# Kernel tuning notes

Measured on AMD Instinct MI355X. Metric: run time of the kernel, lower is better.

## Reference

```python
import jax, jax.numpy as jnp
import numpy as np

B, N, P2, D, L, K = 256, 256, 64, 128, 2, 9  # batch, nodes, patch^2, embed_dim, vig blocks, knn edges
FFN = 4 * D


def _ln(x, g, b, eps=1e-5):
    m = jnp.mean(x, -1, keepdims=True)
    v = jnp.mean((x - m) ** 2, -1, keepdims=True)
    return (x - m) / jnp.sqrt(v + eps) * g + b


def _lrelu(x):
    return jnp.where(x >= 0, x, 0.01 * x)


def _vig_block(x, mask, mf, fc1_w, fc1_b, conv_w, conv_b, fc2_w, fc2_b, f1_w, f1_b, f2_w, f2_b):
    # Grapher: fc1 -> dynamic kNN -> max-relative graph conv -> fc2, residual
    sc = x
    h = x @ fc1_w + fc1_b  # [B,N,D]
    # pairwise squared distances in feature space; masked nodes excluded as neighbors
    x2 = jnp.sum(h * h, -1)
    d2 = x2[:, :, None] + x2[:, None, :] - 2.0 * jnp.einsum('bnd,bmd->bnm', h, h)
    d2 = jnp.where(mask[:, None, :], d2, 1e10)
    _, idx = jax.lax.top_k(-d2, K)  # [B,N,K] nearest-neighbor indices (non-diff)
    Bq, Nq, Dq = h.shape
    hj = jnp.take_along_axis(h, idx.reshape(Bq, Nq * K, 1), axis=1).reshape(Bq, Nq, K, Dq)
    vj = jnp.take_along_axis(mask, idx.reshape(Bq, Nq * K), axis=1).reshape(Bq, Nq, K)
    rel = jnp.where(vj[..., None], hj - h[:, :, None, :], -1e9)
    mrel = jnp.where(vj.any(2)[..., None], rel.max(2), 0.0)  # max-relative aggregation
    h = _lrelu(jnp.concatenate([h, mrel], -1) @ conv_w + conv_b)
    x = (h @ fc2_w + fc2_b) + sc
    # FFN, residual (drop_path = identity at eval)
    sc = x
    x = _lrelu(x @ f1_w + f1_b) @ f2_w + f2_b + sc
    return x * mf


def setup_inputs() -> dict:
    key = jax.random.key(0)
    ks = jax.random.split(key, 32)
    s = 0.02
    d = {
        'nodes_batch': jax.random.normal(ks[0], (B, N, P2), jnp.float32),
        'node_mask': jax.random.randint(ks[1], (B, N), 0, 2) > 0,
        'emb_w1': jax.random.normal(ks[2], (P2, 2 * D), jnp.float32) * s,
        'emb_b1': jnp.zeros((2 * D,), jnp.float32),
        'emb_ln1_g': jnp.ones((2 * D,), jnp.float32),
        'emb_ln1_b': jnp.zeros((2 * D,), jnp.float32),
        'emb_w2': jax.random.normal(ks[3], (2 * D, D), jnp.float32) * s,
        'emb_b2': jnp.zeros((D,), jnp.float32),
        'emb_ln2_g': jnp.ones((D,), jnp.float32),
        'emb_ln2_b': jnp.zeros((D,), jnp.float32),
        'vig_fc1_w': jax.random.normal(ks[4], (L, D, D), jnp.float32) * s,
        'vig_fc1_b': jnp.zeros((L, D), jnp.float32),
        'vig_conv_w': jax.random.normal(ks[5], (L, 2 * D, D), jnp.float32) * s,
        'vig_conv_b': jnp.zeros((L, D), jnp.float32),
        'vig_fc2_w': jax.random.normal(ks[6], (L, D, D), jnp.float32) * s,
        'vig_fc2_b': jnp.zeros((L, D), jnp.float32),
        'vig_ffn1_w': jax.random.normal(ks[7], (L, D, FFN), jnp.float32) * s,
        'vig_ffn1_b': jnp.zeros((L, FFN), jnp.float32),
        'vig_ffn2_w': jax.random.normal(ks[8], (L, FFN, D), jnp.float32) * s,
        'vig_ffn2_b': jnp.zeros((L, D), jnp.float32),
        'out_w1': jax.random.normal(ks[9], (D, 512), jnp.float32) * s,
        'out_b1': jnp.zeros((512,), jnp.float32),
        'out_w2': jax.random.normal(ks[10], (512, 2048), jnp.float32) * s,
        'out_b2': jnp.zeros((2048,), jnp.float32),
    }
    return d


def reference(nodes_batch, node_mask, emb_w1, emb_b1, emb_ln1_g, emb_ln1_b, emb_w2, emb_b2,
              emb_ln2_g, emb_ln2_b, vig_fc1_w, vig_fc1_b, vig_conv_w, vig_conv_b,
              vig_fc2_w, vig_fc2_b, vig_ffn1_w, vig_ffn1_b, vig_ffn2_w, vig_ffn2_b,
              out_w1, out_b1, out_w2, out_b2):
    mf = node_mask[..., None].astype(nodes_batch.dtype)  # [B,N,1]
    # node embed MLP
    x = _lrelu(_ln(nodes_batch @ emb_w1 + emb_b1, emb_ln1_g, emb_ln1_b))
    x = _ln(x @ emb_w2 + emb_b2, emb_ln2_g, emb_ln2_b)
    x = x * mf
    for l in range(L):
        x = _vig_block(x, node_mask, mf,
                       vig_fc1_w[l], vig_fc1_b[l], vig_conv_w[l], vig_conv_b[l],
                       vig_fc2_w[l], vig_fc2_b[l], vig_ffn1_w[l], vig_ffn1_b[l],
                       vig_ffn2_w[l], vig_ffn2_b[l])
    # masked mean pool
    sum_feat = (x * mf).sum(1)
    num_feat = jnp.maximum(mf.sum(1), 1.0)
    g = sum_feat / num_feat
    return _lrelu(g @ out_w1 + out_b1) @ out_w2 + out_b2
```

## Files before the change

kernel.cpp:

```cpp
#include <hip/hip_runtime.h>
#include <cstdint>

#define BB    256
#define NNODE 256
#define PP2   64
#define DD    128
#define LLAY  2
#define KNN   9
#define FFND  512
#define BNROWS (BB*NNODE)

#define LRELU_(v) ((v) >= 0.f ? (v) : 0.01f*(v))

enum { ACT_NONE = 0, ACT_LRELU = 1 };

typedef short  short8_t  __attribute__((ext_vector_type(8)));
typedef float  f32x4     __attribute__((ext_vector_type(4)));
typedef unsigned short us4 __attribute__((ext_vector_type(4)));
typedef unsigned short us8 __attribute__((ext_vector_type(8)));

__device__ inline unsigned short f2bf(float x) {
    unsigned u = __float_as_uint(x);
    unsigned r = (u + 0x7FFFu + ((u >> 16) & 1u)) >> 16;
    return (unsigned short)r;
}
__device__ inline float bf2f(unsigned short h) {
    return __uint_as_float(((unsigned)h) << 16);
}

__device__ inline void gload16(const void* src, void* dst) {
    __builtin_amdgcn_global_load_lds(
        (const __attribute__((address_space(1))) void*)src,
        (__attribute__((address_space(3))) void*)dst, 16, 0, 0);
}

template<int ROWS, int WAVES>
__device__ inline void stage64g(const unsigned short* __restrict__ g, size_t rowbase,
                                int Kel, int k0, unsigned short* lds, int w, int lane)
{
    constexpr int PER = (ROWS*128/1024) / WAVES;
    #pragma unroll
    for (int i = 0; i < PER; ++i) {
        const int inst = w + i*WAVES;
        const unsigned o  = (unsigned)inst*1024u + (unsigned)lane*16u;
        const int      r  = (int)(o >> 7);
        const unsigned cb = o & 127u;
        const unsigned cs = cb ^ ((unsigned)(r & 7) << 4);
        gload16((const char*)(g + (rowbase + (size_t)r)*(size_t)Kel + k0) + cs,
                (char*)lds + (size_t)inst*1024u);
    }
}

__device__ inline short8_t frag64(const unsigned short* lds, int r, int cb) {
    return *reinterpret_cast<const short8_t*>(
        (const char*)lds + (size_t)r*128 + (unsigned)(cb ^ ((r & 7) << 4)));
}

__device__ inline us8 read8sw(const unsigned short* lds, int r, unsigned cb) {
    return *reinterpret_cast<const us8*>(
        (const char*)lds + (size_t)r*128 + (cb ^ ((unsigned)(r & 7) << 4)));
}

__device__ inline unsigned grp16_min_u32(unsigned v) {
    unsigned t;
    t = (unsigned)__builtin_amdgcn_update_dpp(-1, (int)v, 0xB1,  0xF, 0xF, false); v = t < v ? t : v;
    t = (unsigned)__builtin_amdgcn_update_dpp(-1, (int)v, 0x4E,  0xF, 0xF, false); v = t < v ? t : v;
    t = (unsigned)__builtin_amdgcn_update_dpp(-1, (int)v, 0x124, 0xF, 0xF, false); v = t < v ? t : v;
    t = (unsigned)__builtin_amdgcn_update_dpp(-1, (int)v, 0x128, 0xF, 0xF, false); v = t < v ? t : v;
    return v;
}

__device__ inline float dpp_rowsum16(float v) {
    float t;
    t = __uint_as_float((unsigned)__builtin_amdgcn_update_dpp(0, (int)__float_as_uint(v), 0x111, 0xF, 0xF, false)); v += t;
    t = __uint_as_float((unsigned)__builtin_amdgcn_update_dpp(0, (int)__float_as_uint(v), 0x112, 0xF, 0xF, false)); v += t;
    t = __uint_as_float((unsigned)__builtin_amdgcn_update_dpp(0, (int)__float_as_uint(v), 0x114, 0xF, 0xF, false)); v += t;
    t = __uint_as_float((unsigned)__builtin_amdgcn_update_dpp(0, (int)__float_as_uint(v), 0x118, 0xF, 0xF, false)); v += t;
    return v;
}

#define WAITB0  { asm volatile("s_waitcnt vmcnt(0)" ::: "memory");  __builtin_amdgcn_s_barrier(); asm volatile("" ::: "memory"); }
#define WAITB2  { asm volatile("s_waitcnt vmcnt(2)" ::: "memory");  __builtin_amdgcn_s_barrier(); asm volatile("" ::: "memory"); }
#define WAITB4  { asm volatile("s_waitcnt vmcnt(4)" ::: "memory");  __builtin_amdgcn_s_barrier(); asm volatile("" ::: "memory"); }
#define WAITB2L { asm volatile("s_waitcnt vmcnt(2) lgkmcnt(0)" ::: "memory"); __builtin_amdgcn_s_barrier(); asm volatile("" ::: "memory"); }

template<int ACT, bool RES, bool MASK, bool OUTF, bool OUTB, bool OUTS>
__global__ __launch_bounds__(256)
void bgemm_k(const unsigned short* __restrict__ A,
             const unsigned short* __restrict__ W,
             const float* __restrict__ bias,
             const float* __restrict__ resp,
             const int* __restrict__ mask,
             float* __restrict__ Cf, unsigned short* __restrict__ Cb,
             unsigned short* Ohi, unsigned short* Olo,
             int M, int N, int K)
{
    __shared__ __align__(16) unsigned short As[128*64];
    __shared__ __align__(16) unsigned short Bs[128*64];

    const int tid  = threadIdx.x;
    const int lane = tid & 63;
    const int w    = tid >> 6;
    const int wr   = w >> 1, wc = w & 1;
    const int row0 = blockIdx.x * 128;
    const int col0 = blockIdx.y * 128;
    const int l15  = lane & 15;
    const int ko   = lane >> 4;

    f32x4 acc[4][4];
    #pragma unroll
    for (int m = 0; m < 4; ++m)
        #pragma unroll
        for (int n = 0; n < 4; ++n) acc[m][n] = (f32x4){0.f,0.f,0.f,0.f};

    for (int k0 = 0; k0 < K; k0 += 64) {
        stage64g<128,4>(A, (size_t)row0, K, k0, As, w, lane);
        stage64g<128,4>(W, (size_t)col0, K, k0, Bs, w, lane);
        __syncthreads();
        #pragma unroll
        for (int ks = 0; ks < 2; ++ks) {
            short8_t aF[4], bF[4];
            #pragma unroll
            for (int m = 0; m < 4; ++m)
                aF[m] = frag64(As, wr*64 + m*16 + l15, ks*64 + ko*16);
            #pragma unroll
            for (int n = 0; n < 4; ++n)
                bF[n] = frag64(Bs, wc*64 + n*16 + l15, ks*64 + ko*16);
            #pragma unroll
            for (int m = 0; m < 4; ++m)
                #pragma unroll
                for (int n = 0; n < 4; ++n)
                    acc[m][n] = __builtin_amdgcn_mfma_f32_16x16x32_bf16(aF[m], bF[n], acc[m][n], 0, 0, 0);
        }
        __syncthreads();
    }

    #pragma unroll
    for (int m = 0; m < 4; ++m) {
        const int rbase = row0 + wr*64 + m*16 + ko*4;
        #pragma unroll
        for (int n = 0; n < 4; ++n) {
            const int col = col0 + wc*64 + n*16 + l15;
            const float bv = bias[col];
            #pragma unroll
            for (int r = 0; r < 4; ++r) {
                const int row = rbase + r;
                float v = acc[m][n][r] + bv;
                if constexpr (ACT == ACT_LRELU) v = LRELU_(v);
                if constexpr (RES)  v += resp[(size_t)row*N + col];
                if constexpr (MASK) v *= (mask[row] != 0) ? 1.f : 0.f;
                if constexpr (OUTF) Cf[(size_t)row*N + col] = v;
                if constexpr (OUTB) Cb[(size_t)row*N + col] = f2bf(v);
                if constexpr (OUTS) {
                    unsigned short h = f2bf(v);
                    Ohi[(size_t)row*N + col] = h;
                    Olo[(size_t)row*N + col] = f2bf(v - bf2f(h));
                }
            }
        }
    }
}

template<int WR, int WC, bool DO_LRELU, bool MASKMUL, int MODE, bool AF32>
__global__ __launch_bounds__(WR*WC*64)
void bgemm_ln_k(const void* __restrict__ Ap,
                const unsigned short* __restrict__ W,
                const float* __restrict__ bias,
                const float* __restrict__ gam,
                const float* __restrict__ bet,
                const int* __restrict__ mask,
                void* __restrict__ outv,
                unsigned short* __restrict__ ohi, unsigned short* __restrict__ olo,
                int K)
{
    constexpr int BM = WR*64;
    constexpr int BN = WC*64;
    constexpr int THREADS = WR*WC*64;
    constexpr int WAVES = THREADS/64;
    __shared__ __align__(16) unsigned short As[BM*64];
    __shared__ __align__(16) unsigned short Bs[BN*64];
    __shared__ float red_s[WC][BM];
    __shared__ float red_q[WC][BM];
    __shared__ float mu_l[BM];
    __shared__ float rs_l[BM];

    const int tid  = threadIdx.x;
    const int lane = tid & 63;
    const int w    = tid >> 6;
    const int wr   = w / WC, wc = w % WC;
    const int row0 = blockIdx.x * BM;
    const int l15  = lane & 15;
    const int ko   = lane >> 4;

    f32x4 acc[4][4];
    #pragma unroll
    for (int m = 0; m < 4; ++m)
        #pragma unroll
        for (int n = 0; n < 4; ++n) acc[m][n] = (f32x4){0.f,0.f,0.f,0.f};

    for (int k0 = 0; k0 < K; k0 += 64) {
        if constexpr (AF32) {
            const float* Af = (const float*)Ap;
            constexpr int CH = (BM*8)/THREADS;
            #pragma unroll
            for (int i = 0; i < CH; ++i) {
                const int q = i*THREADS + tid;
                const unsigned o  = (unsigned)q*16u;
                const int      r  = (int)(o >> 7);
                const unsigned cb = o & 127u;
                const unsigned cs = cb ^ ((unsigned)(r & 7) << 4);
                const float* src = Af + (size_t)(row0 + r)*K + k0 + (cs >> 1);
                const float4 f0 = *reinterpret_cast<const float4*>(src);
                const float4 f1 = *reinterpret_cast<const float4*>(src + 4);
                short8_t v;
                v[0]=(short)f2bf(f0.x); v[1]=(short)f2bf(f0.y); v[2]=(short)f2bf(f0.z); v[3]=(short)f2bf(f0.w);
                v[4]=(short)f2bf(f1.x); v[5]=(short)f2bf(f1.y); v[6]=(short)f2bf(f1.z); v[7]=(short)f2bf(f1.w);
                *reinterpret_cast<short8_t*>((char*)As + o) = v;
            }
        } else {
            stage64g<BM,WAVES>((const unsigned short*)Ap, (size_t)row0, K, k0, As, w, lane);
        }
        stage64g<BN,WAVES>(W, 0, K, k0, Bs, w, lane);
        __syncthreads();
        #pragma unroll
        for (int ks = 0; ks < 2; ++ks) {
            short8_t aF[4], bF[4];
            #pragma unroll
            for (int m = 0; m < 4; ++m)
                aF[m] = frag64(As, wr*64 + m*16 + l15, ks*64 + ko*16);
            #pragma unroll
            for (int n = 0; n < 4; ++n)
                bF[n] = frag64(Bs, wc*64 + n*16 + l15, ks*64 + ko*16);
            #pragma unroll
            for (int m = 0; m < 4; ++m)
                #pragma unroll
                for (int n = 0; n < 4; ++n)
                    acc[m][n] = __builtin_amdgcn_mfma_f32_16x16x32_bf16(aF[m], bF[n], acc[m][n], 0, 0, 0);
        }
        __syncthreads();
    }

    float bv[4];
    #pragma unroll
    for (int n = 0; n < 4; ++n) bv[n] = bias[wc*64 + n*16 + l15];
    #pragma unroll
    for (int m = 0; m < 4; ++m)
        #pragma unroll
        for (int n = 0; n < 4; ++n)
            #pragma unroll
            for (int r = 0; r < 4; ++r) acc[m][n][r] += bv[n];

    #pragma unroll
    for (int m = 0; m < 4; ++m) {
        #pragma unroll
        for (int r = 0; r < 4; ++r) {
            float s = acc[m][0][r] + acc[m][1][r] + acc[m][2][r] + acc[m][3][r];
            float q = acc[m][0][r]*acc[m][0][r] + acc[m][1][r]*acc[m][1][r]
                    + acc[m][2][r]*acc[m][2][r] + acc[m][3][r]*acc[m][3][r];
            s = dpp_rowsum16(s);
            q = dpp_rowsum16(q);
            if (l15 == 15) {
                int rl = wr*64 + m*16 + ko*4 + r;
                red_s[wc][rl] = s;
                red_q[wc][rl] = q;
            }
        }
    }
    __syncthreads();
    if (tid < BM) {
        float s = 0.f, q = 0.f;
        #pragma unroll
        for (int c2 = 0; c2 < WC; ++c2) { s += red_s[c2][tid]; q += red_q[c2][tid]; }
        float mu  = s * (1.0f/BN);
        float var = q * (1.0f/BN) - mu*mu;
        mu_l[tid] = mu;
        rs_l[tid] = rsqrtf(fmaxf(var, 0.f) + 1e-5f);
    }
    __syncthreads();

    float gm[4], bt[4];
    #pragma unroll
    for (int n = 0; n < 4; ++n) {
        int col = wc*64 + n*16 + l15;
        gm[n] = gam[col]; bt[n] = bet[col];
    }
    #pragma unroll
    for (int m = 0; m < 4; ++m) {
        #pragma unroll
        for (int r = 0; r < 4; ++r) {
            const int rl  = wr*64 + m*16 + ko*4 + r;
            const int row = row0 + rl;
            const float mu = mu_l[rl], rs = rs_l[rl];
            float mf = 1.f;
            if constexpr (MASKMUL) mf = (mask[row] != 0) ? 1.f : 0.f;
            #pragma unroll
            for (int n = 0; n < 4; ++n) {
                const int col = wc*64 + n*16 + l15;
                float y = (acc[m][n][r] - mu) * rs * gm[n] + bt[n];
                if constexpr (DO_LRELU) y = LRELU_(y);
                if constexpr (MASKMUL)  y *= mf;
                if constexpr (MODE == 1) {
                    ((unsigned short*)outv)[(size_t)row*BN + col] = f2bf(y);
                } else {
                    unsigned short h = f2bf(y);
                    ohi[(size_t)row*BN + col] = h;
                    olo[(size_t)row*BN + col] = f2bf(y - bf2f(h));
                }
            }
        }
    }
}

__global__ __launch_bounds__(1024)
void fc1_dist_topk_gather_k(const unsigned short* __restrict__ xhi,
                            const unsigned short* __restrict__ xlo,
                            const unsigned short* __restrict__ Whi,
                            const unsigned short* __restrict__ Wlo,
                            const float* __restrict__ fc1b,
                            const int* __restrict__ mask,
                            unsigned short* __restrict__ cat)
{
    __shared__ __align__(16) unsigned short BUF[4][NNODE*64];
    __shared__ __align__(16) unsigned short Ws[128*64];
    __shared__ float x2s[NNODE];
    __shared__ unsigned char idx_s[NNODE*KNN];
    __shared__ unsigned char msk_s[NNODE];

    const int b    = blockIdx.x;
    const int tid  = threadIdx.x;
    const int lane = tid & 63;
    const int w    = tid >> 6;
    const int l15  = lane & 15;
    const int g    = lane >> 4;

    const unsigned short* Xhi = xhi + (size_t)b*NNODE*DD;
    const unsigned short* Xlo = xlo + (size_t)b*NNODE*DD;
    const int* mkb = mask + b*NNODE;

    stage64g<NNODE,16>(Xhi, 0, DD, 0,  &BUF[0][0], w, lane);
    stage64g<NNODE,16>(Xhi, 0, DD, 64, &BUF[1][0], w, lane);
    stage64g<NNODE,16>(Xlo, 0, DD, 0,  &BUF[2][0], w, lane);
    stage64g<NNODE,16>(Xlo, 0, DD, 64, &BUF[3][0], w, lane);
    if (tid < NNODE) msk_s[tid] = (mkb[tid] != 0) ? 1 : 0;
    __syncthreads();

    const int arow = w*16 + l15;

    f32x4 hacc[8];
    #pragma unroll
    for (int n = 0; n < 8; ++n) hacc[n] = (f32x4){0.f,0.f,0.f,0.f};

    #pragma unroll
    for (int wp = 0; wp < 4; ++wp) {
        const unsigned short* Wsrc = (wp < 2) ? Whi : Wlo;
        const int kt = wp & 1;
        stage64g<128,16>(Wsrc, 0, DD, kt*64, Ws, w, lane);
        __syncthreads();
        const int nAv = (wp < 2) ? 2 : 1;
        for (int av = 0; av < nAv; ++av) {
            const unsigned short* At = (av == 0) ? &BUF[kt][0] : &BUF[2+kt][0];
            #pragma unroll
            for (int ks = 0; ks < 2; ++ks) {
                short8_t aF = frag64(At, arow, ks*64 + g*16);
                #pragma unroll
                for (int n = 0; n < 8; ++n) {
                    short8_t bF = frag64(Ws, n*16 + l15, ks*64 + g*16);
                    hacc[n] = __builtin_amdgcn_mfma_f32_16x16x32_bf16(aF, bF, hacc[n], 0, 0, 0);
                }
            }
        }
        __syncthreads();
    }

    {
        float qr[4] = {0.f, 0.f, 0.f, 0.f};
        #pragma unroll
        for (int n = 0; n < 8; ++n) {
            const int col = n*16 + l15;
            const float bv = fc1b[col];
            const int kt = col >> 6;
            const unsigned bc = (unsigned)((col & 63) * 2);
            #pragma unroll
            for (int r = 0; r < 4; ++r) {
                const int row = w*16 + g*4 + r;
                float v = hacc[n][r] + bv;
                unsigned short hh = f2bf(v);
                unsigned short hl = f2bf(v - bf2f(hh));
                const unsigned off = (unsigned)(row*128) + (bc ^ ((unsigned)(row & 7) << 4));
                *(unsigned short*)((char*)&BUF[kt][0]   + off) = hh;
                *(unsigned short*)((char*)&BUF[2+kt][0] + off) = hl;
                float vv = bf2f(hh) + bf2f(hl);
                qr[r] += vv*vv;
            }
        }
        #pragma unroll
        for (int r = 0; r < 4; ++r) {
            float q = dpp_rowsum16(qr[r]);
            if (l15 == 15) x2s[w*16 + g*4 + r] = q;
        }
    }
    __syncthreads();

    f32x4 acc[16];
    #pragma unroll
    for (int n = 0; n < 16; ++n) acc[n] = (f32x4){0.f,0.f,0.f,0.f};

    __builtin_amdgcn_s_setprio(1);
    #pragma unroll
    for (int kt = 0; kt < 2; ++kt) {
        #pragma unroll
        for (int ks = 0; ks < 2; ++ks) {
            short8_t aH = frag64(&BUF[kt][0],   arow, ks*64 + g*16);
            short8_t aL = frag64(&BUF[2+kt][0], arow, ks*64 + g*16);
            #pragma unroll
            for (int n = 0; n < 16; ++n) {
                int brow = n*16 + l15;
                short8_t bH = frag64(&BUF[kt][0],   brow, ks*64 + g*16);
                short8_t bL = frag64(&BUF[2+kt][0], brow, ks*64 + g*16);
                acc[n] = __builtin_amdgcn_mfma_f32_16x16x32_bf16(aH, bH, acc[n], 0, 0, 0);
                acc[n] = __builtin_amdgcn_mfma_f32_16x16x32_bf16(aL, bH, acc[n], 0, 0, 0);
                acc[n] = __builtin_amdgcn_mfma_f32_16x16x32_bf16(aH, bL, acc[n], 0, 0, 0);
            }
        }
    }
    __builtin_amdgcn_s_setprio(0);

    float x2c[16]; unsigned mk[16];
    #pragma unroll
    for (int n = 0; n < 16; ++n) {
        int col = n*16 + l15;
        x2c[n] = x2s[col];
        mk[n]  = (unsigned)msk_s[col];
    }

    #pragma unroll
    for (int r = 0; r < 4; ++r) {
        const int rb = w*16 + r;
        if ((msk_s[rb] | msk_s[rb+4] | msk_s[rb+8] | msk_s[rb+12]) == 0) continue;
        const int lrow = w*16 + g*4 + r;
        const float x2r = x2s[lrow];
        unsigned key[16];
        #pragma unroll
        for (int n = 0; n < 16; ++n) {
            float v = x2r + x2c[n] - 2.0f*acc[n][r];
            if (!mk[n]) v = 1e10f;
            unsigned u = __float_as_uint(v);
            u = (u & 0x80000000u) ? ~u : (u | 0x80000000u);
            key[n] = (u & 0xFFFFFF00u) | (unsigned)(n*16 + l15);
        }
        for (int it = 0; it < KNN; ++it) {
            unsigned a0 = key[0]  < key[1]  ? key[0]  : key[1];
            unsigned a1 = key[2]  < key[3]  ? key[2]  : key[3];
            unsigned a2 = key[4]  < key[5]  ? key[4]  : key[5];
            unsigned a3 = key[6]  < key[7]  ? key[6]  : key[7];
            unsigned a4 = key[8]  < key[9]  ? key[8]  : key[9];
            unsigned a5 = key[10] < key[11] ? key[10] : key[11];
            unsigned a6 = key[12] < key[13] ? key[12] : key[13];
            unsigned a7 = key[14] < key[15] ? key[14] : key[15];
            unsigned b0 = a0 < a1 ? a0 : a1;
            unsigned b1 = a2 < a3 ? a2 : a3;
            unsigned b2 = a4 < a5 ? a4 : a5;
            unsigned b3 = a6 < a7 ? a6 : a7;
            unsigned c0 = b0 < b1 ? b0 : b1;
            unsigned c1 = b2 < b3 ? b2 : b3;
            unsigned lmin = c0 < c1 ? c0 : c1;
            unsigned gmin = grp16_min_u32(lmin);
            if (l15 == 0) idx_s[lrow*KNN + it] = (unsigned char)(gmin & 0xFFu);
            #pragma unroll
            for (int n = 0; n < 16; ++n)
                if (key[n] == gmin) key[n] = 0xFFFFFFFFu;
        }
    }

    const int gi = lane & 7;
    const unsigned cb = (unsigned)(gi * 16);
    #pragma unroll
    for (int kt = 0; kt < 2; ++kt) {
        #pragma unroll
        for (int p = 0; p < 2; ++p) {
            const int rl = w*16 + p*8 + (lane >> 3);
            us8 h8 = read8sw(&BUF[kt][0],   rl, cb);
            us8 l8 = read8sw(&BUF[2+kt][0], rl, cb);
            float hi[8], m[8];
            #pragma unroll
            for (int d = 0; d < 8; ++d) { hi[d] = bf2f(h8[d]) + bf2f(l8[d]); m[d] = -1e9f; }
            bool any = false;
            #pragma unroll
            for (int q = 0; q < KNN; ++q) {
                int j = idx_s[rl*KNN + q];
                if (msk_s[j]) {
                    any = true;
                    us8 a = read8sw(&BUF[kt][0],   j, cb);
                    us8 o = read8sw(&BUF[2+kt][0], j, cb);
                    #pragma unroll
                    for (int d = 0; d < 8; ++d)
                        m[d] = fmaxf(m[d], bf2f(a[d]) + bf2f(o[d]));
                }
            }
            us8 o1, o2;
            #pragma unroll
            for (int d = 0; d < 8; ++d) {
                o1[d] = f2bf(hi[d]);
                o2[d] = any ? f2bf(m[d] - hi[d]) : (unsigned short)0;
            }
            const size_t rowbase = (size_t)(b*NNODE + rl)*(2*DD);
            const int c0 = kt*64 + gi*8;
            *reinterpret_cast<us8*>(&cat[rowbase + c0])      = o1;
            *reinterpret_cast<us8*>(&cat[rowbase + DD + c0]) = o2;
        }
    }
}

__global__ __launch_bounds__(512, 2)
void conv_ffn_k(const unsigned short* __restrict__ cat,
                const unsigned short* __restrict__ Wc,
                const float* __restrict__ cb,
                const unsigned short* __restrict__ W2c,
                const float* __restrict__ fb,
                const unsigned short* __restrict__ W1,
                const float* __restrict__ b1,
                const unsigned short* __restrict__ W2f,
                const float* __restrict__ b2,
                const int* __restrict__ mask,
                unsigned short* xhi,
                unsigned short* xlo)
{
    __shared__ __align__(16) unsigned short Bs[3][128*64];
    __shared__ __align__(16) unsigned short h2s[2][128*64];
    __shared__ __align__(16) unsigned short Xs[2][128*64];

    const int tid  = threadIdx.x;
    const int lane = tid & 63;
    const int w    = tid >> 6;
    const int wr   = w >> 2;
    const int wc   = w & 3;
    const int row0 = blockIdx.x * 128;
    const int l15  = lane & 15;
    const int ko   = lane >> 4;

    auto issueB = [&](int t) {
        unsigned short* buf = &Bs[t % 3][0];
        if (t < 4)      stage64g<128,8>(Wc,  0, 256, t*64, buf, w, lane);
        else if (t < 6) stage64g<128,8>(W2c, 0, 128, (t-4)*64, buf, w, lane);
        else {
            int c = (t-6) >> 2, j = (t-6) & 3;
            if (j < 2) stage64g<128,8>(W1, (size_t)(c*128), DD, j*64, buf, w, lane);
            else       stage64g<128,8>(W2f, 0, FFND, c*128 + (j-2)*64, buf, w, lane);
        }
    };

    #define MM8(ATILE, BTILE, ACC)                                              \
        { __builtin_amdgcn_s_setprio(1);                                        \
          _Pragma("unroll")                                                     \
          for (int ks = 0; ks < 2; ++ks) {                                      \
            short8_t aF[4], bF[2];                                              \
            _Pragma("unroll")                                                   \
            for (int m = 0; m < 4; ++m) aF[m] = frag64(ATILE, wr*64 + m*16 + l15, ks*64 + ko*16); \
            _Pragma("unroll")                                                   \
            for (int n = 0; n < 2; ++n) bF[n] = frag64(BTILE, wc*32 + n*16 + l15, ks*64 + ko*16); \
            _Pragma("unroll")                                                   \
            for (int m = 0; m < 4; ++m)                                         \
              _Pragma("unroll")                                                 \
              for (int n = 0; n < 2; ++n)                                       \
                ACC[m][n] = __builtin_amdgcn_mfma_f32_16x16x32_bf16(aF[m], bF[n], ACC[m][n], 0, 0, 0); } \
          __builtin_amdgcn_s_setprio(0); }

    #define H2WRITE(ACC, BPTR, DST)                                             \
        { const int kt_ = wc >> 1;                                              \
          _Pragma("unroll")                                                     \
          for (int n = 0; n < 2; ++n) {                                         \
            const int col_ = wc*32 + n*16 + l15;                                \
            const float bv_ = (BPTR)[col_];                                     \
            const unsigned bc_ = (unsigned)(((wc & 1)*32 + n*16 + l15) * 2);    \
            _Pragma("unroll")                                                   \
            for (int m = 0; m < 4; ++m)                                         \
              _Pragma("unroll")                                                 \
              for (int r = 0; r < 4; ++r) {                                     \
                const int row_ = wr*64 + m*16 + ko*4 + r;                       \
                float v_ = LRELU_(ACC[m][n][r] + bv_);                          \
                *(unsigned short*)((char*)&(DST)[kt_][0] + row_*128             \
                    + (bc_ ^ ((unsigned)(row_ & 7) << 4))) = f2bf(v_); } } }

    stage64g<128,8>(cat, (size_t)row0, 256, 0,  &Xs[0][0], w, lane);
    issueB(0);
    stage64g<128,8>(cat, (size_t)row0, 256, 64, &Xs[1][0], w, lane);
    issueB(1);

    f32x4 accc[4][2];
    #pragma unroll
    for (int m = 0; m < 4; ++m)
        #pragma unroll
        for (int n = 0; n < 2; ++n) accc[m][n] = (f32x4){0.f,0.f,0.f,0.f};

    WAITB4;
    issueB(2);
    MM8(&Xs[0][0], &Bs[0][0], accc);

    WAITB2;
    stage64g<128,8>(cat, (size_t)row0, 256, 128, &Xs[0][0], w, lane);
    issueB(3);
    MM8(&Xs[1][0], &Bs[1][0], accc);

    WAITB2;
    stage64g<128,8>(cat, (size_t)row0, 256, 192, &Xs[1][0], w, lane);
    issueB(4);
    MM8(&Xs[0][0], &Bs[2][0], accc);

    WAITB2;
    issueB(5);
    MM8(&Xs[1][0], &Bs[0][0], accc);
    H2WRITE(accc, cb, h2s);

    f32x4 accx[4][2];
    #pragma unroll
    for (int m = 0; m < 4; ++m)
        #pragma unroll
        for (int n = 0; n < 2; ++n) accx[m][n] = (f32x4){0.f,0.f,0.f,0.f};

    WAITB2L;
    issueB(6);
    MM8(&h2s[0][0], &Bs[1][0], accx);

    WAITB2;
    issueB(7);
    MM8(&h2s[1][0], &Bs[2][0], accx);
    float xn[4][2][4];
    {
        const int kt = wc >> 1;
        #pragma unroll
        for (int n = 0; n < 2; ++n) {
            const int col = wc*32 + n*16 + l15;
            const float bv = fb[col];
            const unsigned bc = (unsigned)(((wc & 1)*32 + n*16 + l15) * 2);
            #pragma unroll
            for (int m = 0; m < 4; ++m) {
                #pragma unroll
                for (int r = 0; r < 4; ++r) {
                    const int row = wr*64 + m*16 + ko*4 + r;
                    const size_t gix = (size_t)(row0 + row)*DD + col;
                    float res = bf2f(xhi[gix]) + bf2f(xlo[gix]);
                    float v = accx[m][n][r] + bv + res;
                    xn[m][n][r] = v;
                    *(unsigned short*)((char*)&Xs[kt][0] + row*128
                        + (bc ^ ((unsigned)(row & 7) << 4))) = f2bf(v);
                }
            }
        }
    }

    f32x4 acc2[4][2];
    #pragma unroll
    for (int m = 0; m < 4; ++m)
        #pragma unroll
        for (int n = 0; n < 2; ++n) acc2[m][n] = (f32x4){0.f,0.f,0.f,0.f};

    #pragma unroll
    for (int c = 0; c < 4; ++c) {
        const int tb = 6 + c*4;
        f32x4 acc1[4][2];
        #pragma unroll
        for (int m = 0; m < 4; ++m)
            #pragma unroll
            for (int n = 0; n < 2; ++n) acc1[m][n] = (f32x4){0.f,0.f,0.f,0.f};

        if (c == 0) { WAITB2L; } else { WAITB2; }
        if (tb+2 <= 21) issueB(tb+2);
        MM8(&Xs[0][0], &Bs[tb % 3][0], acc1);

        WAITB2;
        if (tb+3 <= 21) issueB(tb+3);
        MM8(&Xs[1][0], &Bs[(tb+1) % 3][0], acc1);
        H2WRITE(acc1, b1 + c*128, h2s);

        WAITB2L;
        if (tb+4 <= 21) issueB(tb+4);
        MM8(&h2s[0][0], &Bs[(tb+2) % 3][0], acc2);

        if (c == 3) { WAITB0; } else { WAITB2; }
        if (tb+5 <= 21) issueB(tb+5);
        MM8(&h2s[1][0], &Bs[(tb+3) % 3][0], acc2);
    }

    #pragma unroll
    for (int m = 0; m < 4; ++m) {
        const int rbase = row0 + wr*64 + m*16 + ko*4;
        #pragma unroll
        for (int n = 0; n < 2; ++n) {
            const int col = wc*32 + n*16 + l15;
            const float bv = b2[col];
            #pragma unroll
            for (int r = 0; r < 4; ++r) {
                const int row = rbase + r;
                float v = acc2[m][n][r] + bv + xn[m][n][r];
                v *= (mask[row] != 0) ? 1.f : 0.f;
                unsigned short h = f2bf(v);
                xhi[(size_t)row*DD + col] = h;
                xlo[(size_t)row*DD + col] = f2bf(v - bf2f(h));
            }
        }
    }
    #undef MM8
    #undef H2WRITE
}

__global__ __launch_bounds__(128)
void pool_k(const unsigned short* __restrict__ xhi, const unsigned short* __restrict__ xlo,
            const int* __restrict__ mask,
            float* __restrict__ g, unsigned short* __restrict__ gbf)
{
    const int b = blockIdx.x, c = threadIdx.x;
    float s = 0.f; int cnt = 0;
    for (int n = 0; n < NNODE; ++n) {
        const size_t ix = ((size_t)b*NNODE + n)*DD + c;
        s += bf2f(xhi[ix]) + bf2f(xlo[ix]);
        cnt += (mask[b*NNODE + n] != 0) ? 1 : 0;
    }
    float v = s / fmaxf((float)cnt, 1.0f);
    g[b*DD + c] = v;
    gbf[b*DD + c] = f2bf(v);
}

__global__ __launch_bounds__(256)
void prep_all_k(const float* __restrict__ emb_w1, const float* __restrict__ emb_w2,
                const float* __restrict__ conv_w, const float* __restrict__ fc2_w,
                const float* __restrict__ f1_w,   const float* __restrict__ f2_w,
                const float* __restrict__ fc1_w,  const float* __restrict__ ow1,
                const float* __restrict__ ow2,
                unsigned short* __restrict__ emb_w1t, unsigned short* __restrict__ emb_w2t,
                unsigned short* __restrict__ conv_wt, unsigned short* __restrict__ fc2_wt,
                unsigned short* __restrict__ ffn1_wt, unsigned short* __restrict__ ffn2_wt,
                unsigned short* __restrict__ fc1_wthi, unsigned short* __restrict__ fc1_wtlo,
                unsigned short* __restrict__ ow1t, unsigned short* __restrict__ ow2t)
{
    __shared__ float tile[32][33];
    const int tx = threadIdx.x & 31, ty = threadIdx.x >> 5;

    int bid = blockIdx.x;
    const float* src = nullptr; unsigned short* dst = nullptr; unsigned short* dlo = nullptr;
    int K = 0, N = 0;
    do {
        if (bid < 16)  { src = emb_w1; dst = emb_w1t; K = 64;  N = 256; break; }  bid -= 16;
        if (bid < 32)  { src = emb_w2; dst = emb_w2t; K = 256; N = 128; break; }  bid -= 32;
        if (bid < 64)  { int l = bid >> 5; bid &= 31;
                         src = conv_w + (size_t)l*256*128; dst = conv_wt + (size_t)l*128*256;
                         K = 256; N = 128; break; }                               bid -= 64;
        if (bid < 32)  { int l = bid >> 4; bid &= 15;
                         src = fc2_w + (size_t)l*128*128; dst = fc2_wt + (size_t)l*128*128;
                         K = 128; N = 128; break; }                               bid -= 32;
        if (bid < 128) { int l = bid >> 6; bid &= 63;
                         src = f1_w + (size_t)l*128*512; dst = ffn1_wt + (size_t)l*512*128;
                         K = 128; N = 512; break; }                               bid -= 128;
        if (bid < 128) { int l = bid >> 6; bid &= 63;
                         src = f2_w + (size_t)l*512*128; dst = ffn2_wt + (size_t)l*128*512;
                         K = 512; N = 128; break; }                               bid -= 128;
        if (bid < 32)  { int l = bid >> 4; bid &= 15;
                         src = fc1_w + (size_t)l*128*128;
                         dst = fc1_wthi + (size_t)l*128*128; dlo = fc1_wtlo + (size_t)l*128*128;
                         K = 128; N = 128; break; }                               bid -= 32;
        if (bid < 64)  { src = ow1; dst = ow1t; K = 128; N = 512; break; }        bid -= 64;
        { src = ow2; dst = ow2t; K = 512; N = 2048; }
    } while (0);

    const int nbx = N / 32;
    const int bx = bid % nbx, by = bid / nbx;
    const int k0 = by*32, n0 = bx*32;

    #pragma unroll
    for (int i = ty; i < 32; i += 8)
        tile[i][tx] = src[(size_t)(k0+i)*N + n0+tx];
    __syncthreads();
    #pragma unroll
    for (int i = ty; i < 32; i += 8) {
        float v = tile[tx][i];
        unsigned short h = f2bf(v);
        dst[(size_t)(n0+i)*K + k0+tx] = h;
        if (dlo) dlo[(size_t)(n0+i)*K + k0+tx] = f2bf(v - bf2f(h));
    }
}

extern "C" void kernel_launch(void* const* d_in, const int* in_sizes, int n_in,
                              void* d_out, int out_size, void* d_ws, size_t ws_size,
                              hipStream_t stream)
{
    const float* nodes  = (const float*)d_in[0];
    const int*   maskp  = (const int*)  d_in[1];
    const float* emb_w1 = (const float*)d_in[2];
    const float* emb_b1 = (const float*)d_in[3];
    const float* ln1_g  = (const float*)d_in[4];
    const float* ln1_b  = (const float*)d_in[5];
    const float* emb_w2 = (const float*)d_in[6];
    const float* emb_b2 = (const float*)d_in[7];
    const float* ln2_g  = (const float*)d_in[8];
    const float* ln2_b  = (const float*)d_in[9];
    const float* fc1_w  = (const float*)d_in[10];
    const float* fc1_b  = (const float*)d_in[11];
    const float* conv_w = (const float*)d_in[12];
    const float* conv_b = (const float*)d_in[13];
    const float* fc2_w  = (const float*)d_in[14];
    const float* fc2_b  = (const float*)d_in[15];
    const float* f1_w   = (const float*)d_in[16];
    const float* f1_b   = (const float*)d_in[17];
    const float* f2_w   = (const float*)d_in[18];
    const float* f2_b   = (const float*)d_in[19];
    const float* ow1    = (const float*)d_in[20];
    const float* ob1    = (const float*)d_in[21];
    const float* ow2    = (const float*)d_in[22];
    const float* ob2    = (const float*)d_in[23];
    float* out = (float*)d_out;

    char* base = (char*)d_ws;
    char*  H   = base + (size_t)BNROWS*DD*4;
    char*  BIG = H + (size_t)BNROWS*DD*4;
    float*          g     = (float*)(BIG + (size_t)BNROWS*2*DD*4);
    unsigned short* g_bf  = (unsigned short*)(g + BB*DD);
    unsigned short* hid2_bf = g_bf + BB*DD;
    unsigned short* wbuf  = hid2_bf + BB*FFND;

    unsigned short* x_hi   = (unsigned short*)H;
    unsigned short* x_lo   = x_hi + (size_t)BNROWS*DD;
    unsigned short* t256_bf= (unsigned short*)base;
    unsigned short* cat_bf = (unsigned short*)BIG;

    unsigned short* emb_w1t  = wbuf;
    unsigned short* emb_w2t  = emb_w1t + 256*64;
    unsigned short* conv_wt  = emb_w2t + 128*256;
    unsigned short* fc2_wt   = conv_wt + 2*128*256;
    unsigned short* ffn1_wt  = fc2_wt  + 2*128*128;
    unsigned short* ffn2_wt  = ffn1_wt + 2*512*128;
    unsigned short* fc1_wthi = ffn2_wt + 2*128*512;
    unsigned short* fc1_wtlo = fc1_wthi + 2*128*128;
    unsigned short* ow1t     = fc1_wtlo + 2*128*128;
    unsigned short* ow2t     = ow1t + 512*128;

    const dim3 blk(256);

    prep_all_k<<<1520, blk, 0, stream>>>(
        emb_w1, emb_w2, conv_w, fc2_w, f1_w, f2_w, fc1_w, ow1, ow2,
        emb_w1t, emb_w2t, conv_wt, fc2_wt, ffn1_wt, ffn2_wt,
        fc1_wthi, fc1_wtlo, ow1t, ow2t);

    bgemm_ln_k<2,4,true,false,1,true>
        <<<dim3(BNROWS/128), dim3(512), 0, stream>>>
        (nodes, emb_w1t, emb_b1, ln1_g, ln1_b, nullptr, t256_bf, nullptr, nullptr, PP2);
    bgemm_ln_k<2,2,false,true,2,false>
        <<<dim3(BNROWS/128), dim3(256), 0, stream>>>
        (t256_bf, emb_w2t, emb_b2, ln2_g, ln2_b, maskp, nullptr, x_hi, x_lo, 2*DD);

    for (int l = 0; l < LLAY; ++l) {
        const float* fc1b = fc1_b + (size_t)l*DD;
        const float* cb   = conv_b + (size_t)l*DD;
        const float* fc2b = fc2_b + (size_t)l*DD;
        const float* b1   = f1_b + (size_t)l*FFND;
        const float* b2   = f2_b + (size_t)l*DD;

        fc1_dist_topk_gather_k<<<dim3(BB), dim3(1024), 0, stream>>>
            (x_hi, x_lo, fc1_wthi + (size_t)l*DD*DD, fc1_wtlo + (size_t)l*DD*DD,
             fc1b, maskp, cat_bf);
        conv_ffn_k<<<dim3(BNROWS/128), dim3(512), 0, stream>>>
            (cat_bf, conv_wt + (size_t)l*DD*2*DD, cb,
             fc2_wt + (size_t)l*DD*DD, fc2b,
             ffn1_wt + (size_t)l*FFND*DD, b1,
             ffn2_wt + (size_t)l*DD*FFND, b2, maskp,
             x_hi, x_lo);
    }

    pool_k<<<BB, 128, 0, stream>>>(x_hi, x_lo, maskp, g, g_bf);
    bgemm_k<ACT_LRELU,false,false,false,true,false>
        <<<dim3(BB/128, 512/128), blk, 0, stream>>>
        (g_bf, ow1t, ob1, nullptr, nullptr, nullptr, hid2_bf, nullptr, nullptr, BB, 512, DD);
    bgemm_k<ACT_NONE,false,false,true,false,false>
        <<<dim3(BB/128, 2048/128), blk, 0, stream>>>
        (hid2_bf, ow2t, ob2, nullptr, nullptr, out, nullptr, nullptr, nullptr, BB, 2048, 512);
}
```

Before: 276.3 us.

## Halve conv_ffn row tile to 64 and raise occupancy to four blocks per CU

The fused conv+FFN kernel now processes 64 rows per block instead of 128. Each of the 8 waves owns a 16-column strip across all 64 rows, so accumulators shrink and launch bounds allow 4 blocks per CU. The Xs and h2s LDS buffers are halved and the wait counts are adjusted for the smaller staging. The aim is better latency hiding and more blocks in flight. In exchange, every weight tile is reloaded by twice as many blocks, which doubles weight traffic and lowers MFMA reuse per B fragment.

```diff
diff --git a/kernel.cpp b/kernel.cpp
--- a/kernel.cpp
+++ b/kernel.cpp
@@ -81,7 +81,7 @@
 
 #define WAITB0  { asm volatile("s_waitcnt vmcnt(0)" ::: "memory");  __builtin_amdgcn_s_barrier(); asm volatile("" ::: "memory"); }
 #define WAITB2  { asm volatile("s_waitcnt vmcnt(2)" ::: "memory");  __builtin_amdgcn_s_barrier(); asm volatile("" ::: "memory"); }
-#define WAITB4  { asm volatile("s_waitcnt vmcnt(4)" ::: "memory");  __builtin_amdgcn_s_barrier(); asm volatile("" ::: "memory"); }
+#define WAITB3  { asm volatile("s_waitcnt vmcnt(3)" ::: "memory");  __builtin_amdgcn_s_barrier(); asm volatile("" ::: "memory"); }
 #define WAITB2L { asm volatile("s_waitcnt vmcnt(2) lgkmcnt(0)" ::: "memory"); __builtin_amdgcn_s_barrier(); asm volatile("" ::: "memory"); }
 
 template<int ACT, bool RES, bool MASK, bool OUTF, bool OUTB, bool OUTS>
@@ -511,7 +511,7 @@
     }
 }
 
-__global__ __launch_bounds__(512, 2)
+__global__ __launch_bounds__(512, 4)
 void conv_ffn_k(const unsigned short* __restrict__ cat,
                 const unsigned short* __restrict__ Wc,
                 const float* __restrict__ cb,
@@ -526,15 +526,13 @@
                 unsigned short* xlo)
 {
     __shared__ __align__(16) unsigned short Bs[3][128*64];
-    __shared__ __align__(16) unsigned short h2s[2][128*64];
-    __shared__ __align__(16) unsigned short Xs[2][128*64];
+    __shared__ __align__(16) unsigned short h2s[2][64*64];
+    __shared__ __align__(16) unsigned short Xs[2][64*64];
 
     const int tid  = threadIdx.x;
     const int lane = tid & 63;
     const int w    = tid >> 6;
-    const int wr   = w >> 2;
-    const int wc   = w & 3;
-    const int row0 = blockIdx.x * 128;
+    const int row0 = blockIdx.x * 64;
     const int l15  = lane & 15;
     const int ko   = lane >> 4;
 
@@ -553,56 +551,49 @@
         { __builtin_amdgcn_s_setprio(1);                                        \
           _Pragma("unroll")                                                     \
           for (int ks = 0; ks < 2; ++ks) {                                      \
-            short8_t aF[4], bF[2];                                              \
+            short8_t aF[4], bF;                                                 \
             _Pragma("unroll")                                                   \
-            for (int m = 0; m < 4; ++m) aF[m] = frag64(ATILE, wr*64 + m*16 + l15, ks*64 + ko*16); \
-            _Pragma("unroll")                                                   \
-            for (int n = 0; n < 2; ++n) bF[n] = frag64(BTILE, wc*32 + n*16 + l15, ks*64 + ko*16); \
+            for (int m = 0; m < 4; ++m) aF[m] = frag64(ATILE, m*16 + l15, ks*64 + ko*16); \
+            bF = frag64(BTILE, w*16 + l15, ks*64 + ko*16);                      \
             _Pragma("unroll")                                                   \
             for (int m = 0; m < 4; ++m)                                         \
-              _Pragma("unroll")                                                 \
-              for (int n = 0; n < 2; ++n)                                       \
-                ACC[m][n] = __builtin_amdgcn_mfma_f32_16x16x32_bf16(aF[m], bF[n], ACC[m][n], 0, 0, 0); } \
+              ACC[m] = __builtin_amdgcn_mfma_f32_16x16x32_bf16(aF[m], bF, ACC[m], 0, 0, 0); } \
           __builtin_amdgcn_s_setprio(0); }
 
     #define H2WRITE(ACC, BPTR, DST)                                             \
-        { const int kt_ = wc >> 1;                                              \
+        { const int kt_ = w >> 2;                                               \
+          const int col_ = w*16 + l15;                                          \
+          const float bv_ = (BPTR)[col_];                                       \
+          const unsigned bc_ = (unsigned)(((w & 3)*16 + l15) * 2);              \
           _Pragma("unroll")                                                     \
-          for (int n = 0; n < 2; ++n) {                                         \
-            const int col_ = wc*32 + n*16 + l15;                                \
-            const float bv_ = (BPTR)[col_];                                     \
-            const unsigned bc_ = (unsigned)(((wc & 1)*32 + n*16 + l15) * 2);    \
+          for (int m = 0; m < 4; ++m)                                           \
             _Pragma("unroll")                                                   \
-            for (int m = 0; m < 4; ++m)                                         \
-              _Pragma("unroll")                                                 \
-              for (int r = 0; r < 4; ++r) {                                     \
-                const int row_ = wr*64 + m*16 + ko*4 + r;                       \
-                float v_ = LRELU_(ACC[m][n][r] + bv_);                          \
-                *(unsigned short*)((char*)&(DST)[kt_][0] + row_*128             \
-                    + (bc_ ^ ((unsigned)(row_ & 7) << 4))) = f2bf(v_); } } }
-
-    stage64g<128,8>(cat, (size_t)row0, 256, 0,  &Xs[0][0], w, lane);
+            for (int r = 0; r < 4; ++r) {                                       \
+              const int row_ = m*16 + ko*4 + r;                                 \
+              float v_ = LRELU_(ACC[m][r] + bv_);                               \
+              *(unsigned short*)((char*)&(DST)[kt_][0] + row_*128               \
+                  + (bc_ ^ ((unsigned)(row_ & 7) << 4))) = f2bf(v_); } }
+
+    stage64g<64,8>(cat, (size_t)row0, 256, 0,  &Xs[0][0], w, lane);
     issueB(0);
-    stage64g<128,8>(cat, (size_t)row0, 256, 64, &Xs[1][0], w, lane);
+    stage64g<64,8>(cat, (size_t)row0, 256, 64, &Xs[1][0], w, lane);
     issueB(1);
 
-    f32x4 accc[4][2];
-    #pragma unroll
-    for (int m = 0; m < 4; ++m)
-        #pragma unroll
-        for (int n = 0; n < 2; ++n) accc[m][n] = (f32x4){0.f,0.f,0.f,0.f};
-
-    WAITB4;
+    f32x4 accc[4];
+    #pragma unroll
+    for (int m = 0; m < 4; ++m) accc[m] = (f32x4){0.f,0.f,0.f,0.f};
+
+    WAITB3;
     issueB(2);
     MM8(&Xs[0][0], &Bs[0][0], accc);
 
     WAITB2;
-    stage64g<128,8>(cat, (size_t)row0, 256, 128, &Xs[0][0], w, lane);
+    stage64g<64,8>(cat, (size_t)row0, 256, 128, &Xs[0][0], w, lane);
     issueB(3);
     MM8(&Xs[1][0], &Bs[1][0], accc);
 
     WAITB2;
-    stage64g<128,8>(cat, (size_t)row0, 256, 192, &Xs[1][0], w, lane);
+    stage64g<64,8>(cat, (size_t)row0, 256, 192, &Xs[1][0], w, lane);
     issueB(4);
     MM8(&Xs[0][0], &Bs[2][0], accc);
 
@@ -611,11 +602,9 @@
     MM8(&Xs[1][0], &Bs[0][0], accc);
     H2WRITE(accc, cb, h2s);
 
-    f32x4 accx[4][2];
-    #pragma unroll
-    for (int m = 0; m < 4; ++m)
-        #pragma unroll
-        for (int n = 0; n < 2; ++n) accx[m][n] = (f32x4){0.f,0.f,0.f,0.f};
+    f32x4 accx[4];
+    #pragma unroll
+    for (int m = 0; m < 4; ++m) accx[m] = (f32x4){0.f,0.f,0.f,0.f};
 
     WAITB2L;
     issueB(6);
@@ -624,44 +613,37 @@
     WAITB2;
     issueB(7);
     MM8(&h2s[1][0], &Bs[2][0], accx);
-    float xn[4][2][4];
+    float xn[4][4];
     {
-        const int kt = wc >> 1;
-        #pragma unroll
-        for (int n = 0; n < 2; ++n) {
-            const int col = wc*32 + n*16 + l15;
-            const float bv = fb[col];
-            const unsigned bc = (unsigned)(((wc & 1)*32 + n*16 + l15) * 2);
-            #pragma unroll
-            for (int m = 0; m < 4; ++m) {
-                #pragma unroll
-                for (int r = 0; r < 4; ++r) {
-                    const int row = wr*64 + m*16 + ko*4 + r;
-                    const size_t gix = (size_t)(row0 + row)*DD + col;
-                    float res = bf2f(xhi[gix]) + bf2f(xlo[gix]);
-                    float v = accx[m][n][r] + bv + res;
-                    xn[m][n][r] = v;
-                    *(unsigned short*)((char*)&Xs[kt][0] + row*128
-                        + (bc ^ ((unsigned)(row & 7) << 4))) = f2bf(v);
-                }
-            }
-        }
-    }
-
-    f32x4 acc2[4][2];
-    #pragma unroll
-    for (int m = 0; m < 4; ++m)
-        #pragma unroll
-        for (int n = 0; n < 2; ++n) acc2[m][n] = (f32x4){0.f,0.f,0.f,0.f};
+        const int kt = w >> 2;
+        const int col = w*16 + l15;
+        const float bv = fb[col];
+        const unsigned bc = (unsigned)(((w & 3)*16 + l15) * 2);
+        #pragma unroll
+        for (int m = 0; m < 4; ++m) {
+            #pragma unroll
+            for (int r = 0; r < 4; ++r) {
+                const int row = m*16 + ko*4 + r;
+                const size_t gix = (size_t)(row0 + row)*DD + col;
+                float res = bf2f(xhi[gix]) + bf2f(xlo[gix]);
+                float v = accx[m][r] + bv + res;
+                xn[m][r] = v;
+                *(unsigned short*)((char*)&Xs[kt][0] + row*128
+                    + (bc ^ ((unsigned)(row & 7) << 4))) = f2bf(v);
+            }
+        }
+    }
+
+    f32x4 acc2[4];
+    #pragma unroll
+    for (int m = 0; m < 4; ++m) acc2[m] = (f32x4){0.f,0.f,0.f,0.f};
 
     #pragma unroll
     for (int c = 0; c < 4; ++c) {
         const int tb = 6 + c*4;
-        f32x4 acc1[4][2];
-        #pragma unroll
-        for (int m = 0; m < 4; ++m)
-            #pragma unroll
-            for (int n = 0; n < 2; ++n) acc1[m][n] = (f32x4){0.f,0.f,0.f,0.f};
+        f32x4 acc1[4];
+        #pragma unroll
+        for (int m = 0; m < 4; ++m) acc1[m] = (f32x4){0.f,0.f,0.f,0.f};
 
         if (c == 0) { WAITB2L; } else { WAITB2; }
         if (tb+2 <= 21) issueB(tb+2);
@@ -681,17 +663,16 @@
         MM8(&h2s[1][0], &Bs[(tb+3) % 3][0], acc2);
     }
 
-    #pragma unroll
-    for (int m = 0; m < 4; ++m) {
-        const int rbase = row0 + wr*64 + m*16 + ko*4;
-        #pragma unroll
-        for (int n = 0; n < 2; ++n) {
-            const int col = wc*32 + n*16 + l15;
-            const float bv = b2[col];
+    {
+        const int col = w*16 + l15;
+        const float bv = b2[col];
+        #pragma unroll
+        for (int m = 0; m < 4; ++m) {
+            const int rbase = row0 + m*16 + ko*4;
             #pragma unroll
             for (int r = 0; r < 4; ++r) {
                 const int row = rbase + r;
-                float v = acc2[m][n][r] + bv + xn[m][n][r];
+                float v = acc2[m][r] + bv + xn[m][r];
                 v *= (mask[row] != 0) ? 1.f : 0.f;
                 unsigned short h = f2bf(v);
                 xhi[(size_t)row*DD + col] = h;
@@ -856,7 +837,7 @@
         fc1_dist_topk_gather_k<<<dim3(BB), dim3(1024), 0, stream>>>
             (x_hi, x_lo, fc1_wthi + (size_t)l*DD*DD, fc1_wtlo + (size_t)l*DD*DD,
              fc1b, maskp, cat_bf);
-        conv_ffn_k<<<dim3(BNROWS/128), dim3(512), 0, stream>>>
+        conv_ffn_k<<<dim3(BNROWS/64), dim3(512), 0, stream>>>
             (cat_bf, conv_wt + (size_t)l*DD*2*DD, cb,
              fc2_wt + (size_t)l*DD*DD, fc2b,
              ffn1_wt + (size_t)l*FFND*DD, b1,
```

Result: faster. 261.7 us (-5.3%).
